# Performance work log

Hardware: AMD Instinct MI355X
Metric: run time of the kernel (lower is better)

The kernel has to match this reference:

```python
import jax, jax.numpy as jnp
import numpy as np

NUM_MODELS = 4
B = 16384
HIDDEN = 512
QDIM = 256
LAST_HIDDEN = 256
UW = 0.1          # uncertainty_weight
EPS = 1e-5        # LayerNorm eps (torch default)
FEAT_DIMS = [1024, 768, 512, 640]


def _linear(x, W, b):
    return x @ W.T + b


def _layernorm(h, g, b):
    mu = jnp.mean(h, axis=-1, keepdims=True)
    var = jnp.mean((h - mu) ** 2, axis=-1, keepdims=True)
    return (h - mu) * jax.lax.rsqrt(var + EPS) * g + b


def setup_inputs() -> dict:
    key = jax.random.key(0)
    ks = jax.random.split(key, 40)
    inp = {}
    for i, d in enumerate(FEAT_DIMS):
        inp[f"feat{i}"] = jax.random.normal(ks[i], (B, d), jnp.float32)
        inp[f"W_intra{i}"] = jax.random.normal(ks[4 + i], (HIDDEN, d), jnp.float32) / np.sqrt(d)
        inp[f"b_intra{i}"] = jnp.zeros((HIDDEN,), jnp.float32)
    inp["pred_scores"] = jax.random.uniform(ks[8], (B, NUM_MODELS), jnp.float32)
    inp["pred_vars"] = jax.random.uniform(ks[9], (B, NUM_MODELS), jnp.float32)
    inp["ln_g"] = jnp.ones((HIDDEN,), jnp.float32)
    inp["ln_b"] = jnp.zeros((HIDDEN,), jnp.float32)
    inp["Wq"] = jax.random.normal(ks[10], (QDIM, HIDDEN), jnp.float32) / np.sqrt(HIDDEN)
    inp["bq"] = jnp.zeros((QDIM,), jnp.float32)
    inp["Wk"] = jax.random.normal(ks[11], (QDIM, HIDDEN), jnp.float32) / np.sqrt(HIDDEN)
    inp["bk"] = jnp.zeros((QDIM,), jnp.float32)
    inp["Wv"] = jax.random.normal(ks[12], (QDIM, HIDDEN), jnp.float32) / np.sqrt(HIDDEN)
    inp["bv"] = jnp.zeros((QDIM,), jnp.float32)
    d1 = NUM_MODELS * QDIM + NUM_MODELS
    inp["W1"] = jax.random.normal(ks[13], (LAST_HIDDEN, d1), jnp.float32) / np.sqrt(d1)
    inp["b1"] = jnp.zeros((LAST_HIDDEN,), jnp.float32)
    inp["Wfc"] = jax.random.normal(ks[14], (1, LAST_HIDDEN), jnp.float32) / np.sqrt(LAST_HIDDEN)
    inp["bfc"] = jnp.zeros((1,), jnp.float32)
    return inp


def _forward(feats, pred_scores, pred_vars, W_intras, b_intras,
             ln_g, ln_b, Wq, bq, Wk, bk, Wv, bv, W1, b1, Wfc, bfc):
    # per-model branch: Linear -> ReLU -> (dropout=id) -> ReLU -> LayerNorm
    hiddens = []
    for i in range(NUM_MODELS):
        h = jax.nn.relu(_linear(feats[i], W_intras[i], b_intras[i]))
        h = jax.nn.relu(h)  # second relu after dropout (identity in eval)
        hiddens.append(_layernorm(h, ln_g, ln_b))
    H = jnp.stack(hiddens, axis=1)  # (B, M, HIDDEN)

    # cross-attention with uncertainty; NOTE source bug: key = drop(q) => keys == queries
    q = jnp.einsum('bmh,qh->bmq', H, Wq) + bq          # (B, M, Q)
    k = q                                              # faithful to `key = self.drop(q)`
    v = jnp.einsum('bmh,qh->bmq', H, Wv) + bv          # (B, M, Q)

    scores = jnp.einsum('biq,bjq->bij', q, k)          # (B, M, M)
    vars_ = pred_vars[:, None, :] + pred_vars[:, :, None]  # vars[b,i,j] = v[b,j] + v[b,i]
    scores = jax.nn.softmax(scores - UW * vars_, axis=-1)
    z = jnp.einsum('bij,bjq->biq', scores, v).reshape(B, NUM_MODELS * QDIM)

    out = jnp.concatenate([z, pred_scores], axis=-1)
    out = _linear(out, W1, b1)
    logits = _linear(out, Wfc, bfc)
    return jax.nn.sigmoid(logits)  # (B, 1)


def reference(feat0, feat1, feat2, feat3,
              W_intra0, b_intra0, W_intra1, b_intra1,
              W_intra2, b_intra2, W_intra3, b_intra3,
              pred_scores, pred_vars, ln_g, ln_b,
              Wq, bq, Wk, bk, Wv, bv, W1, b1, Wfc, bfc):
    feats = [feat0, feat1, feat2, feat3]
    W_intras = [W_intra0, W_intra1, W_intra2, W_intra3]
    b_intras = [b_intra0, b_intra1, b_intra2, b_intra3]
    return _forward(feats, pred_scores, pred_vars, W_intras, b_intras,
                    ln_g, ln_b, Wq, bq, Wk, bk, Wv, bv, W1, b1, Wfc, bfc)
```

## Files before the change

### kernel.cpp

```cpp
#include <hip/hip_runtime.h>
#include <hip/hip_bf16.h>


typedef __bf16 bf16;
typedef __bf16 bf16x4_t __attribute__((ext_vector_type(4)));
typedef __bf16 bf16x8_t __attribute__((ext_vector_type(8)));
typedef float  f32x4_t  __attribute__((ext_vector_type(4)));

__device__ __forceinline__ bf16x8_t cvt8(f32x4_t a, f32x4_t b) {
  bf16x8_t r;
  r[0] = (bf16)a[0]; r[1] = (bf16)a[1]; r[2] = (bf16)a[2]; r[3] = (bf16)a[3];
  r[4] = (bf16)b[0]; r[5] = (bf16)b[1]; r[6] = (bf16)b[2]; r[7] = (bf16)b[3];
  return r;
}

__device__ __forceinline__ void gl_lds16(const void* g, void* l) {
  __builtin_amdgcn_global_load_lds(
      (const __attribute__((address_space(1))) void*)g,
      (__attribute__((address_space(3))) void*)l, 16, 0, 0);
}

#define SBAR()   __builtin_amdgcn_s_barrier()
#define SCHED0() __builtin_amdgcn_sched_barrier(0)

__device__ __forceinline__ bf16x8_t frag_b16(const bf16* Ts, int row, int c0) {
  const int byte = row * 64 + ((c0 ^ ((row >> 1) & 3)) << 4);
  return *(const bf16x8_t*)((const char*)Ts + byte);
}
__device__ __forceinline__ bf16x8_t frag_f32(const float* Ts, int row, int g) {
  const int p0 = (2 * g)     ^ (row & 7);
  const int p1 = (2 * g + 1) ^ (row & 7);
  f32x4_t lo = *(const f32x4_t*)((const char*)Ts + row * 128 + (p0 << 4));
  f32x4_t hi = *(const f32x4_t*)((const char*)Ts + row * 128 + (p1 << 4));
  return cvt8(lo, hi);
}

__device__ __forceinline__ void stage_f32_512(const float* __restrict__ src, int ld,
                                              int k0, float* lds) {
  const int l = threadIdx.x & 63;
  const int w = threadIdx.x >> 6;
#pragma unroll
  for (int j = 0; j < 2; ++j) {
    const int rb = w * 16 + j * 8;
    const int r  = rb + (l >> 3);
    const int q  = (l & 7) ^ (r & 7);
    gl_lds16(src + (size_t)r * ld + k0 + q * 4, (char*)lds + rb * 128);
  }
}
__device__ __forceinline__ void stage_b512x32(const bf16* __restrict__ src, int ld,
                                              int k0, bf16* lds) {
  const int l = threadIdx.x & 63;
  const int w = threadIdx.x >> 6;
#pragma unroll
  for (int j = 0; j < 4; ++j) {
    const int rb = w * 64 + j * 16;
    const int r  = rb + (l >> 2);
    const int sc = (l & 3) ^ ((r >> 1) & 3);
    gl_lds16(src + (size_t)r * ld + k0 + sc * 8, (char*)lds + rb * 64);
  }
}

__global__ __launch_bounds__(512) void intra_ln_kernel(
    const float* __restrict__ f0, const float* __restrict__ f1,
    const float* __restrict__ f2, const float* __restrict__ f3,
    const bf16* __restrict__ wb0, const bf16* __restrict__ wb1,
    const bf16* __restrict__ wb2, const bf16* __restrict__ wb3,
    const float* __restrict__ bb0, const float* __restrict__ bb1,
    const float* __restrict__ bb2, const float* __restrict__ bb3,
    const float* __restrict__ lng, const float* __restrict__ lnb,
    bf16* __restrict__ Hout) {
  __shared__ __align__(16) char lds[98304];
  const int bid  = blockIdx.x;
  const int p    = bid & 255, half = bid >> 8;
  const int px   = (p & 7) * 32 + (p >> 3);
  int z = px & 3, y = px >> 2;
  if (half) { z ^= 2; y += 64; }
  const float* fp; const bf16* wp; const float* bp; int K;
  switch (z) {
    case 0:  fp = f0; wp = wb0; bp = bb0; K = 1024; break;
    case 1:  fp = f1; wp = wb1; bp = bb1; K = 768;  break;
    case 2:  fp = f2; wp = wb2; bp = bb2; K = 512;  break;
    default: fp = f3; wp = wb3; bp = bb3; K = 640;  break;
  }
  const float* A = fp + (size_t)(y * 128) * K;
  const bf16*  B = wp;
  const int tid = threadIdx.x;
  const int lane = tid & 63;
  const int wid  = tid >> 6;
  const int wm = wid >> 2, wn = wid & 3;
  const int fr = lane & 15, g = lane >> 4;

  f32x4_t acc[4][8];
#pragma unroll
  for (int i = 0; i < 4; ++i)
#pragma unroll
    for (int j = 0; j < 8; ++j) acc[i][j] = (f32x4_t){0.f, 0.f, 0.f, 0.f};

  const int nt = K >> 5;
  char* buf0 = lds;
  char* buf1 = lds + 49152;
  auto stage = [&](int t, char* buf) {
    stage_f32_512(A, K, t * 32, (float*)buf);
    stage_b512x32(B, K, t * 32, (bf16*)(buf + 16384));
  };
  stage(0, buf0);
  stage(1, buf1);
  for (int t = 0; t < nt; ++t) {
    char* cur = (t & 1) ? buf1 : buf0;
    if (t + 1 < nt) asm volatile("s_waitcnt vmcnt(6)" ::: "memory");
    else            asm volatile("s_waitcnt vmcnt(0)" ::: "memory");
    SBAR(); SCHED0();
    __builtin_amdgcn_s_setprio(1);
    {
      const float* Af = (const float*)cur;
      const bf16*  Bb = (const bf16*)(cur + 16384);
      bf16x8_t ar[4], br[8];
#pragma unroll
      for (int mi = 0; mi < 4; ++mi) ar[mi] = frag_f32(Af, wm * 64 + mi * 16 + fr, g);
#pragma unroll
      for (int ni = 0; ni < 8; ++ni) br[ni] = frag_b16(Bb, wn * 128 + ni * 16 + fr, g);
#pragma unroll
      for (int mi = 0; mi < 4; ++mi)
#pragma unroll
        for (int ni = 0; ni < 8; ++ni)
          acc[mi][ni] = __builtin_amdgcn_mfma_f32_16x16x32_bf16(ar[mi], br[ni], acc[mi][ni], 0, 0, 0);
    }
    __builtin_amdgcn_s_setprio(0);
    SCHED0(); SBAR();
    if (t + 2 < nt) stage(t + 2, cur);
  }

  float* part  = (float*)lds;
  float* muinv = (float*)(lds + 4096);
  float bv8[8];
#pragma unroll
  for (int ni = 0; ni < 8; ++ni) bv8[ni] = bp[wn * 128 + ni * 16 + fr];
#pragma unroll
  for (int mi = 0; mi < 4; ++mi)
#pragma unroll
    for (int j = 0; j < 4; ++j) {
      float s = 0.f, s2 = 0.f;
#pragma unroll
      for (int ni = 0; ni < 8; ++ni) {
        float v = fmaxf(acc[mi][ni][j] + bv8[ni], 0.f);
        s += v; s2 += v * v;
      }
#pragma unroll
      for (int off = 1; off < 16; off <<= 1) {
        s += __shfl_xor(s, off); s2 += __shfl_xor(s2, off);
      }
      if (fr == 0) {
        const int rl = mi * 16 + 4 * g + j;
        part[(wid * 64 + rl) * 2]     = s;
        part[(wid * 64 + rl) * 2 + 1] = s2;
      }
    }
  __syncthreads();
  if (tid < 128) {
    const int wmt = tid >> 6, rl = tid & 63;
    float s = 0.f, s2 = 0.f;
#pragma unroll
    for (int q = 0; q < 4; ++q) {
      s  += part[((wmt * 4 + q) * 64 + rl) * 2];
      s2 += part[((wmt * 4 + q) * 64 + rl) * 2 + 1];
    }
    const float mu  = s * (1.f / 512.f);
    const float var = s2 * (1.f / 512.f) - mu * mu;
    muinv[tid * 2]     = mu;
    muinv[tid * 2 + 1] = rsqrtf(var + 1e-5f);
  }
  __syncthreads();
  float gg[8], be[8];
#pragma unroll
  for (int ni = 0; ni < 8; ++ni) {
    const int col = wn * 128 + ni * 16 + fr;
    gg[ni] = lng[col]; be[ni] = lnb[col];
  }
#pragma unroll
  for (int mi = 0; mi < 4; ++mi)
#pragma unroll
    for (int j = 0; j < 4; ++j) {
      const int row = wm * 64 + mi * 16 + 4 * g + j;
      const float mu  = muinv[row * 2];
      const float inv = muinv[row * 2 + 1];
      bf16* hp = Hout + (size_t)(y * 128 + row) * 2048 + z * 512;
#pragma unroll
      for (int ni = 0; ni < 8; ++ni) {
        float v = fmaxf(acc[mi][ni][j] + bv8[ni], 0.f);
        hp[wn * 128 + ni * 16 + fr] = (bf16)((v - mu) * inv * gg[ni] + be[ni]);
      }
    }
}

__device__ __forceinline__ void stage_b16(const bf16* __restrict__ src, int ld,
                                          int k0, bf16* lds) {
  const int l = threadIdx.x & 63;
  const int w = threadIdx.x >> 6;
#pragma unroll
  for (int j = 0; j < 2; ++j) {
    const int rb = w * 32 + j * 16;
    const int r  = rb + (l >> 2);
    const int sc = (l & 3) ^ ((r >> 1) & 3);
    gl_lds16(src + (size_t)r * ld + k0 + sc * 8, (char*)lds + rb * 64);
  }
}
__device__ __forceinline__ void stage_f32(const float* __restrict__ src, int ld,
                                          int k0, float* lds) {
  const int l = threadIdx.x & 63;
  const int w = threadIdx.x >> 6;
#pragma unroll
  for (int j = 0; j < 4; ++j) {
    const int rb = w * 32 + j * 8;
    const int r  = rb + (l >> 3);
    const int q  = (l & 7) ^ (r & 7);
    gl_lds16(src + (size_t)r * ld + k0 + q * 4, (char*)lds + rb * 128);
  }
}
__device__ __forceinline__ void mfma_deep0(const char* buf, f32x4_t acc[4][4]) {
  const int lane = threadIdx.x & 63;
  const int wid  = threadIdx.x >> 6;
  const int wm = wid >> 1, wn = wid & 1;
  const int fr = lane & 15, g = lane >> 4;
  const bf16*  Ab = (const bf16*)buf;
  const float* Bf = (const float*)(buf + 8192);
  bf16x8_t ar[4], br[4];
#pragma unroll
  for (int mi = 0; mi < 4; ++mi) ar[mi] = frag_b16(Ab, wm * 64 + mi * 16 + fr, g);
#pragma unroll
  for (int ni = 0; ni < 4; ++ni) br[ni] = frag_f32(Bf, wn * 64 + ni * 16 + fr, g);
#pragma unroll
  for (int mi = 0; mi < 4; ++mi)
#pragma unroll
    for (int ni = 0; ni < 4; ++ni)
      acc[mi][ni] = __builtin_amdgcn_mfma_f32_16x16x32_bf16(ar[mi], br[ni], acc[mi][ni], 0, 0, 0);
}
__device__ __forceinline__ void core_deep3_0(const void* A, int lda, const void* B,
                                             int ldb, int K, char* lds,
                                             f32x4_t acc[4][4]) {
  const int nt = K >> 5;
  auto stage = [&](int t, char* buf) {
    stage_b16((const bf16*)A, lda, t * 32, (bf16*)buf);
    stage_f32((const float*)B, ldb, t * 32, (float*)(buf + 8192));
  };
  stage(0, lds); stage(1, lds + 24576); stage(2, lds + 49152);
  int bsel = 0;
  for (int t = 0; t < nt; ++t) {
    const int ahead = nt - 1 - t;
    if (ahead >= 2)      asm volatile("s_waitcnt vmcnt(12)" ::: "memory");
    else if (ahead == 1) asm volatile("s_waitcnt vmcnt(6)"  ::: "memory");
    else                 asm volatile("s_waitcnt vmcnt(0)"  ::: "memory");
    SBAR(); SCHED0();
    __builtin_amdgcn_s_setprio(1);
    mfma_deep0(lds + bsel * 24576, acc);
    __builtin_amdgcn_s_setprio(0);
    SCHED0(); SBAR();
    if (t + 3 < nt) stage(t + 3, lds + bsel * 24576);
    bsel = (bsel == 2) ? 0 : bsel + 1;
  }
}
template<int RELU>
__device__ __forceinline__ void epi_bf16(f32x4_t acc[4][4], bf16* __restrict__ C, int ldc,
                                         const float* __restrict__ bias) {
  const int lane = threadIdx.x & 63;
  const int wid  = threadIdx.x >> 6;
  const int wm = wid >> 1, wn = wid & 1;
  const int fr = lane & 15;
  const int rb = wm * 64 + 4 * (lane >> 4);
  const int cb = wn * 64 + fr;
  float bv[4];
#pragma unroll
  for (int ni = 0; ni < 4; ++ni) bv[ni] = bias[cb + ni * 16];
#pragma unroll
  for (int mi = 0; mi < 4; ++mi)
#pragma unroll
    for (int j = 0; j < 4; ++j)
#pragma unroll
      for (int ni = 0; ni < 4; ++ni) {
        float val = acc[mi][ni][j] + bv[ni];
        if (RELU) val = fmaxf(val, 0.f);
        C[(size_t)(rb + mi * 16 + j) * ldc + cb + ni * 16] = (bf16)val;
      }
}

__global__ __launch_bounds__(256) void qv_kernel(
    const bf16* __restrict__ H, const float* __restrict__ Wq,
    const float* __restrict__ Wv, const float* __restrict__ bq,
    const float* __restrict__ bv, bf16* __restrict__ qvout) {
  __shared__ __align__(16) char lds[73728];
  const int bid = blockIdx.x;
  const int lid = (bid & 7) * 256 + (bid >> 3);
  const int x = lid & 3, y = lid >> 2;
  const float* Wsrc = (x < 2) ? Wq : Wv;
  f32x4_t acc[4][4];
#pragma unroll
  for (int i = 0; i < 4; ++i)
#pragma unroll
    for (int j = 0; j < 4; ++j) acc[i][j] = (f32x4_t){0.f, 0.f, 0.f, 0.f};
  core_deep3_0(H + (size_t)(y * 128) * 512, 512,
               Wsrc + (size_t)((x & 1) * 128) * 512, 512, 512, lds, acc);
  const float* bias = (x < 2) ? bq + x * 128 : bv + (x - 2) * 128;
  epi_bf16<0>(acc, qvout + (size_t)(y * 128) * 512 + x * 128, 512, bias);
}

__global__ __launch_bounds__(256) void w1_kernel(
    const bf16* __restrict__ zb, const float* __restrict__ W1,
    const float* __restrict__ b1, const float* __restrict__ ps,
    float* __restrict__ obuf) {
  __shared__ __align__(16) char lds[73728];
  const int bid = blockIdx.x;
  const int lid = (bid & 7) * 32 + (bid >> 3);
  const int x = lid & 1, y = lid >> 1;
  f32x4_t acc[4][4];
#pragma unroll
  for (int i = 0; i < 4; ++i)
#pragma unroll
    for (int j = 0; j < 4; ++j) acc[i][j] = (f32x4_t){0.f, 0.f, 0.f, 0.f};
  core_deep3_0(zb + (size_t)(y * 128) * 1024, 1024,
               W1 + (size_t)(x * 128) * 1028, 1028, 1024, lds, acc);

  const int lane = threadIdx.x & 63;
  const int wid  = threadIdx.x >> 6;
  const int wm = wid >> 1, wn = wid & 1;
  const int fr = lane & 15;
  const int rb = wm * 64 + 4 * (lane >> 4);
  const int cb = x * 128 + wn * 64 + fr;
  float bv[4], wt[4][4];
#pragma unroll
  for (int ni = 0; ni < 4; ++ni) {
    bv[ni] = b1[cb + ni * 16];
#pragma unroll
    for (int m = 0; m < 4; ++m) wt[ni][m] = W1[(size_t)(cb + ni * 16) * 1028 + 1024 + m];
  }
#pragma unroll
  for (int mi = 0; mi < 4; ++mi)
#pragma unroll
    for (int j = 0; j < 4; ++j) {
      const int r = y * 128 + rb + mi * 16 + j;
      f32x4_t psv = *(const f32x4_t*)(ps + (size_t)r * 4);
#pragma unroll
      for (int ni = 0; ni < 4; ++ni) {
        float val = acc[mi][ni][j] + bv[ni]
                  + psv[0] * wt[ni][0] + psv[1] * wt[ni][1]
                  + psv[2] * wt[ni][2] + psv[3] * wt[ni][3];
        obuf[(size_t)r * 256 + cb + ni * 16] = val;
      }
    }
}

__device__ __forceinline__ void cp8(bf16* d, const float* s) {
  f32x4_t x0 = *(const f32x4_t*)s;
  f32x4_t x1 = *(const f32x4_t*)(s + 4);
  *(bf16x8_t*)d = cvt8(x0, x1);
}
__global__ __launch_bounds__(256) void prep_kernel(
    const float* __restrict__ w0, const float* __restrict__ w1s,
    const float* __restrict__ w2, const float* __restrict__ w3,
    bf16* __restrict__ o0, bf16* __restrict__ o1,
    bf16* __restrict__ o2, bf16* __restrict__ o3) {
  const int t = blockIdx.x * 256 + threadIdx.x;
  if (t < 65536)       { size_t i = (size_t)t * 8;            cp8(o0 + i, w0 + i); }
  else if (t < 114688) { size_t i = (size_t)(t - 65536) * 8;  cp8(o1 + i, w1s + i); }
  else if (t < 147456) { size_t i = (size_t)(t - 114688) * 8; cp8(o2 + i, w2 + i); }
  else                 { size_t i = (size_t)(t - 147456) * 8; cp8(o3 + i, w3 + i); }
}

__global__ __launch_bounds__(256)
void attn_kernel(const bf16* __restrict__ qv, const float* __restrict__ pvars,
                 bf16* __restrict__ z) {
  const int b    = blockIdx.x * 4 + (threadIdx.x >> 6);
  const int lane = threadIdx.x & 63;
  float qf[4][4], vf[4][4];
#pragma unroll
  for (int i = 0; i < 4; ++i) {
    const bf16* row = qv + ((size_t)b * 4 + i) * 512;
    bf16x4_t qq = *(const bf16x4_t*)(row + lane * 4);
    bf16x4_t vv = *(const bf16x4_t*)(row + 256 + lane * 4);
#pragma unroll
    for (int c = 0; c < 4; ++c) { qf[i][c] = (float)qq[c]; vf[i][c] = (float)vv[c]; }
  }
  float s[4][4];
#pragma unroll
  for (int i = 0; i < 4; ++i)
#pragma unroll
    for (int j = 0; j < 4; ++j)
      s[i][j] = qf[i][0] * qf[j][0] + qf[i][1] * qf[j][1] + qf[i][2] * qf[j][2] + qf[i][3] * qf[j][3];
#pragma unroll
  for (int off = 1; off < 64; off <<= 1)
#pragma unroll
    for (int i = 0; i < 4; ++i)
#pragma unroll
      for (int j = 0; j < 4; ++j) s[i][j] += __shfl_xor(s[i][j], off);

  float var4[4];
#pragma unroll
  for (int m = 0; m < 4; ++m) var4[m] = pvars[(size_t)b * 4 + m];
  float w[4][4];
#pragma unroll
  for (int i = 0; i < 4; ++i) {
    float t[4]; float mx = -1e30f;
#pragma unroll
    for (int j = 0; j < 4; ++j) { t[j] = s[i][j] - 0.1f * (var4[i] + var4[j]); mx = fmaxf(mx, t[j]); }
    float sum = 0.f;
#pragma unroll
    for (int j = 0; j < 4; ++j) { t[j] = expf(t[j] - mx); sum += t[j]; }
    const float is = 1.f / sum;
#pragma unroll
    for (int j = 0; j < 4; ++j) w[i][j] = t[j] * is;
  }
#pragma unroll
  for (int i = 0; i < 4; ++i) {
    bf16x4_t zo;
#pragma unroll
    for (int c = 0; c < 4; ++c) {
      float zf = w[i][0] * vf[0][c] + w[i][1] * vf[1][c] + w[i][2] * vf[2][c] + w[i][3] * vf[3][c];
      zo[c] = (bf16)zf;
    }
    *(bf16x4_t*)(z + ((size_t)b * 4 + i) * 256 + lane * 4) = zo;
  }
}

__global__ __launch_bounds__(256)
void fc_kernel(const float* __restrict__ o, const float* __restrict__ wfc,
               const float* __restrict__ bfc, float* __restrict__ out) {
  const int b    = blockIdx.x * 4 + (threadIdx.x >> 6);
  const int lane = threadIdx.x & 63;
  f32x4_t ov = *(const f32x4_t*)(o + (size_t)b * 256 + lane * 4);
  f32x4_t wv = *(const f32x4_t*)(wfc + lane * 4);
  float p = ov[0] * wv[0] + ov[1] * wv[1] + ov[2] * wv[2] + ov[3] * wv[3];
#pragma unroll
  for (int off = 1; off < 64; off <<= 1) p += __shfl_xor(p, off);
  if (lane == 0) {
    const float lg = p + bfc[0];
    out[b] = 1.f / (1.f + expf(-lg));
  }
}

extern "C" void kernel_launch(void* const* d_in, const int* in_sizes, int n_in,
                              void* d_out, int out_size, void* d_ws, size_t ws_size,
                              hipStream_t stream) {
  (void)in_sizes; (void)n_in; (void)out_size; (void)ws_size;
  const float* feat[4] = {(const float*)d_in[0], (const float*)d_in[3],
                          (const float*)d_in[6], (const float*)d_in[9]};
  const float* Wi[4]   = {(const float*)d_in[1], (const float*)d_in[4],
                          (const float*)d_in[7], (const float*)d_in[10]};
  const float* bi[4]   = {(const float*)d_in[2], (const float*)d_in[5],
                          (const float*)d_in[8], (const float*)d_in[11]};
  const float* ps  = (const float*)d_in[12];
  const float* pv  = (const float*)d_in[13];
  const float* lng = (const float*)d_in[14];
  const float* lnb = (const float*)d_in[15];
  const float* Wq  = (const float*)d_in[16];
  const float* bq  = (const float*)d_in[17];
  const float* Wv  = (const float*)d_in[20];
  const float* bvp = (const float*)d_in[21];
  const float* W1  = (const float*)d_in[22];
  const float* b1  = (const float*)d_in[23];
  const float* Wfc = (const float*)d_in[24];
  const float* bfc = (const float*)d_in[25];

  char* ws = (char*)d_ws;
  const size_t MB = 1024 * 1024;
  bf16*  hbuf  = (bf16*)ws;
  bf16*  zbuf  = (bf16*)ws;
  float* obuf  = (float*)(ws + 32 * MB);
  bf16*  wb0   = (bf16*)(ws + 64 * MB);
  bf16*  wb1   = (bf16*)(ws + 65 * MB);
  bf16*  wb2   = (bf16*)(ws + 65 * MB + 786432);
  bf16*  wb3   = (bf16*)(ws + 66 * MB + 262144);
  bf16*  qvout = (bf16*)(ws + 64 * MB);

  hipLaunchKernelGGL(prep_kernel, dim3(736), dim3(256), 0, stream,
                     Wi[0], Wi[1], Wi[2], Wi[3], wb0, wb1, wb2, wb3);
  hipLaunchKernelGGL(intra_ln_kernel, dim3(512), dim3(512), 0, stream,
                     feat[0], feat[1], feat[2], feat[3],
                     wb0, wb1, wb2, wb3, bi[0], bi[1], bi[2], bi[3],
                     lng, lnb, hbuf);
  hipLaunchKernelGGL(qv_kernel, dim3(2048), dim3(256), 0, stream,
                     hbuf, Wq, Wv, bq, bvp, qvout);
  hipLaunchKernelGGL(attn_kernel, dim3(16384 / 4), dim3(256), 0, stream, qvout, pv, zbuf);
  hipLaunchKernelGGL(w1_kernel, dim3(256), dim3(256), 0, stream, zbuf, W1, b1, ps, obuf);
  hipLaunchKernelGGL(fc_kernel, dim3(16384 / 4), dim3(256), 0, stream, obuf, Wfc, bfc, (float*)d_out);
}
```

Measured before the change: 237.9 us.

## Convert fp32 A tile to bf16 in registers before LDS, triple-buffer weights

The fp32 activation tile is now loaded into registers, converted to bf16 and written to a small double-buffered LDS region, instead of being copied as fp32 via direct global-to-LDS loads and converted on every fragment read. Weight tiles move to a three-slot ring buffer so each prefetch lands in a different slot from the one being read. This halves the LDS footprint and read traffic for A and drops repeated conversions, at the cost of register-staged loads that add VGPR pressure and an extra lgkmcnt wait, plus a larger total LDS allocation.

```diff
diff --git a/kernel.cpp b/kernel.cpp
--- a/kernel.cpp
+++ b/kernel.cpp
@@ -35,18 +35,6 @@
   return cvt8(lo, hi);
 }
 
-__device__ __forceinline__ void stage_f32_512(const float* __restrict__ src, int ld,
-                                              int k0, float* lds) {
-  const int l = threadIdx.x & 63;
-  const int w = threadIdx.x >> 6;
-#pragma unroll
-  for (int j = 0; j < 2; ++j) {
-    const int rb = w * 16 + j * 8;
-    const int r  = rb + (l >> 3);
-    const int q  = (l & 7) ^ (r & 7);
-    gl_lds16(src + (size_t)r * ld + k0 + q * 4, (char*)lds + rb * 128);
-  }
-}
 __device__ __forceinline__ void stage_b512x32(const bf16* __restrict__ src, int ld,
                                               int k0, bf16* lds) {
   const int l = threadIdx.x & 63;
@@ -69,7 +57,8 @@
     const float* __restrict__ bb2, const float* __restrict__ bb3,
     const float* __restrict__ lng, const float* __restrict__ lnb,
     bf16* __restrict__ Hout) {
-  __shared__ __align__(16) char lds[98304];
+  __shared__ __align__(16) char lds[114688];
+
   const int bid  = blockIdx.x;
   const int p    = bid & 255, half = bid >> 8;
   const int px   = (p & 7) * 32 + (p >> 3);
@@ -90,6 +79,10 @@
   const int wm = wid >> 2, wn = wid & 3;
   const int fr = lane & 15, g = lane >> 4;
 
+  const int srow = tid >> 2, sq = tid & 3;
+  const float* Af = A + (size_t)srow * K + sq * 8;
+  const int abyte = srow * 64 + ((sq ^ ((srow >> 1) & 3)) << 4);
+
   f32x4_t acc[4][8];
 #pragma unroll
   for (int i = 0; i < 4; ++i)
@@ -97,38 +90,55 @@
     for (int j = 0; j < 8; ++j) acc[i][j] = (f32x4_t){0.f, 0.f, 0.f, 0.f};
 
   const int nt = K >> 5;
-  char* buf0 = lds;
-  char* buf1 = lds + 49152;
-  auto stage = [&](int t, char* buf) {
-    stage_f32_512(A, K, t * 32, (float*)buf);
-    stage_b512x32(B, K, t * 32, (bf16*)(buf + 16384));
-  };
-  stage(0, buf0);
-  stage(1, buf1);
-  for (int t = 0; t < nt; ++t) {
-    char* cur = (t & 1) ? buf1 : buf0;
-    if (t + 1 < nt) asm volatile("s_waitcnt vmcnt(6)" ::: "memory");
-    else            asm volatile("s_waitcnt vmcnt(0)" ::: "memory");
-    SBAR(); SCHED0();
-    __builtin_amdgcn_s_setprio(1);
-    {
-      const float* Af = (const float*)cur;
-      const bf16*  Bb = (const bf16*)(cur + 16384);
-      bf16x8_t ar[4], br[8];
-#pragma unroll
-      for (int mi = 0; mi < 4; ++mi) ar[mi] = frag_f32(Af, wm * 64 + mi * 16 + fr, g);
-#pragma unroll
-      for (int ni = 0; ni < 8; ++ni) br[ni] = frag_b16(Bb, wn * 128 + ni * 16 + fr, g);
-#pragma unroll
-      for (int mi = 0; mi < 4; ++mi)
-#pragma unroll
-        for (int ni = 0; ni < 8; ++ni)
-          acc[mi][ni] = __builtin_amdgcn_mfma_f32_16x16x32_bf16(ar[mi], br[ni], acc[mi][ni], 0, 0, 0);
-    }
-    __builtin_amdgcn_s_setprio(0);
-    SCHED0(); SBAR();
-    if (t + 2 < nt) stage(t + 2, cur);
-  }
+
+  stage_b512x32(B, K, 0, (bf16*)(lds));
+  f32x4_t aA0 = *(const f32x4_t*)(Af + 0);
+  f32x4_t aA1 = *(const f32x4_t*)(Af + 4);
+  stage_b512x32(B, K, 32, (bf16*)(lds + 32768));
+  f32x4_t aB0, aB1;
+
+  int bcur = 0;
+#define INTRA_ITER(T, C0, C1, N0, N1)                                         \
+  {                                                                           \
+    const int t_ = (T);                                                       \
+    if (t_ < nt - 1) asm volatile("s_waitcnt vmcnt(4)" ::: "memory");         \
+    else             asm volatile("s_waitcnt vmcnt(0)" ::: "memory");         \
+    *(bf16x8_t*)(lds + 98304 + (t_ & 1) * 8192 + abyte) = cvt8(C0, C1);       \
+    asm volatile("s_waitcnt lgkmcnt(0)" ::: "memory");                        \
+    SBAR(); SCHED0();                                                         \
+    if (t_ + 1 < nt) {                                                        \
+      N0 = *(const f32x4_t*)(Af + (t_ + 1) * 32);                             \
+      N1 = *(const f32x4_t*)(Af + (t_ + 1) * 32 + 4);                         \
+    }                                                                         \
+    SCHED0();                                                                 \
+    __builtin_amdgcn_s_setprio(1);                                            \
+    {                                                                         \
+      const bf16* Ac = (const bf16*)(lds + 98304 + (t_ & 1) * 8192);          \
+      const bf16* Bc = (const bf16*)(lds + bcur * 32768);                     \
+      bf16x8_t ar[4], br[8];                                                  \
+      _Pragma("unroll")                                                       \
+      for (int mi = 0; mi < 4; ++mi) ar[mi] = frag_b16(Ac, wm * 64 + mi * 16 + fr, g); \
+      _Pragma("unroll")                                                       \
+      for (int ni = 0; ni < 8; ++ni) br[ni] = frag_b16(Bc, wn * 128 + ni * 16 + fr, g); \
+      _Pragma("unroll")                                                       \
+      for (int mi = 0; mi < 4; ++mi)                                          \
+        _Pragma("unroll")                                                     \
+        for (int ni = 0; ni < 8; ++ni)                                        \
+          acc[mi][ni] = __builtin_amdgcn_mfma_f32_16x16x32_bf16(ar[mi], br[ni], acc[mi][ni], 0, 0, 0); \
+    }                                                                         \
+    __builtin_amdgcn_s_setprio(0);                                            \
+    SCHED0(); SBAR();                                                         \
+    const int bn_ = (bcur == 2) ? 0 : bcur + 1;          \
+    const int b2_ = (bn_ == 2) ? 0 : bn_ + 1;           \
+    if (t_ + 2 < nt) stage_b512x32(B, K, (t_ + 2) * 32, (bf16*)(lds + b2_ * 32768)); \
+    bcur = bn_;                                                               \
+  }
+
+  for (int t = 0; t < nt; t += 2) {
+    INTRA_ITER(t,     aA0, aA1, aB0, aB1)
+    INTRA_ITER(t + 1, aB0, aB1, aA0, aA1)
+  }
+#undef INTRA_ITER
 
   float* part  = (float*)lds;
   float* muinv = (float*)(lds + 4096);
```

Measured after the change: 228.7 us. 1.04x faster.

## Double block size in intra_ln kernel and triple-buffer weight staging

Applied to the files above, without the earlier changes.

The fused intra-linear + LayerNorm kernel now runs 1024 threads (16 waves) per block instead of 512, so each wave computes a 64x64 tile rather than 64x128, which halves accumulator registers per wave. Weight tiles are triple-buffered and feature tiles double-buffered in a 128 KB LDS allocation. Loads for the next steps are issued before the wait, with the vmcnt counts adjusted to match. This aims to raise latency hiding and overlap of global loads with MFMA work, at the cost of more LDS, barrier overhead across more waves, and lower per-wave fragment reuse.

```diff
diff --git a/kernel.cpp b/kernel.cpp
--- a/kernel.cpp
+++ b/kernel.cpp
@@ -35,32 +35,7 @@
   return cvt8(lo, hi);
 }
 
-__device__ __forceinline__ void stage_f32_512(const float* __restrict__ src, int ld,
-                                              int k0, float* lds) {
-  const int l = threadIdx.x & 63;
-  const int w = threadIdx.x >> 6;
-#pragma unroll
-  for (int j = 0; j < 2; ++j) {
-    const int rb = w * 16 + j * 8;
-    const int r  = rb + (l >> 3);
-    const int q  = (l & 7) ^ (r & 7);
-    gl_lds16(src + (size_t)r * ld + k0 + q * 4, (char*)lds + rb * 128);
-  }
-}
-__device__ __forceinline__ void stage_b512x32(const bf16* __restrict__ src, int ld,
-                                              int k0, bf16* lds) {
-  const int l = threadIdx.x & 63;
-  const int w = threadIdx.x >> 6;
-#pragma unroll
-  for (int j = 0; j < 4; ++j) {
-    const int rb = w * 64 + j * 16;
-    const int r  = rb + (l >> 2);
-    const int sc = (l & 3) ^ ((r >> 1) & 3);
-    gl_lds16(src + (size_t)r * ld + k0 + sc * 8, (char*)lds + rb * 64);
-  }
-}
-
-__global__ __launch_bounds__(512) void intra_ln_kernel(
+__global__ __launch_bounds__(1024, 4) void intra_ln_kernel(
     const float* __restrict__ f0, const float* __restrict__ f1,
     const float* __restrict__ f2, const float* __restrict__ f3,
     const bf16* __restrict__ wb0, const bf16* __restrict__ wb1,
@@ -69,7 +44,8 @@
     const float* __restrict__ bb2, const float* __restrict__ bb3,
     const float* __restrict__ lng, const float* __restrict__ lnb,
     bf16* __restrict__ Hout) {
-  __shared__ __align__(16) char lds[98304];
+  __shared__ __align__(16) char lds[131072];
+
   const int bid  = blockIdx.x;
   const int p    = bid & 255, half = bid >> 8;
   const int px   = (p & 7) * 32 + (p >> 3);
@@ -84,65 +60,79 @@
   }
   const float* A = fp + (size_t)(y * 128) * K;
   const bf16*  B = wp;
-  const int tid = threadIdx.x;
+  const int tid  = threadIdx.x;
   const int lane = tid & 63;
   const int wid  = tid >> 6;
-  const int wm = wid >> 2, wn = wid & 3;
+  const int wm = wid >> 3, wn = wid & 7;
   const int fr = lane & 15, g = lane >> 4;
 
-  f32x4_t acc[4][8];
+  f32x4_t acc[4][4];
 #pragma unroll
   for (int i = 0; i < 4; ++i)
 #pragma unroll
-    for (int j = 0; j < 8; ++j) acc[i][j] = (f32x4_t){0.f, 0.f, 0.f, 0.f};
+    for (int j = 0; j < 4; ++j) acc[i][j] = (f32x4_t){0.f, 0.f, 0.f, 0.f};
 
   const int nt = K >> 5;
-  char* buf0 = lds;
-  char* buf1 = lds + 49152;
-  auto stage = [&](int t, char* buf) {
-    stage_f32_512(A, K, t * 32, (float*)buf);
-    stage_b512x32(B, K, t * 32, (bf16*)(buf + 16384));
+
+  auto stageA = [&](int t) {
+    const int rb = wid * 8;
+    const int r  = rb + (lane >> 3);
+    const int q  = (lane & 7) ^ (r & 7);
+    gl_lds16(A + (size_t)r * K + t * 32 + q * 4,
+             lds + 98304 + (t & 1) * 16384 + rb * 128);
   };
-  stage(0, buf0);
-  stage(1, buf1);
+  auto stageB = [&](int t) {
+#pragma unroll
+    for (int j = 0; j < 2; ++j) {
+      const int rb = wid * 32 + j * 16;
+      const int r  = rb + (lane >> 2);
+      const int sc = (lane & 3) ^ ((r >> 1) & 3);
+      gl_lds16(B + (size_t)r * K + t * 32 + sc * 8,
+               lds + (t % 3) * 32768 + rb * 64);
+    }
+  };
+
+  stageA(0); stageB(0); stageB(1);
   for (int t = 0; t < nt; ++t) {
-    char* cur = (t & 1) ? buf1 : buf0;
-    if (t + 1 < nt) asm volatile("s_waitcnt vmcnt(6)" ::: "memory");
-    else            asm volatile("s_waitcnt vmcnt(0)" ::: "memory");
+    if (t + 1 < nt) stageA(t + 1);
+    if (t + 2 < nt) stageB(t + 2);
+    const int rem = ((t + 1 < nt) ? 3 : 0) + ((t + 2 < nt) ? 2 : 0);
+    if (rem == 5)      asm volatile("s_waitcnt vmcnt(5)" ::: "memory");
+    else if (rem == 3) asm volatile("s_waitcnt vmcnt(3)" ::: "memory");
+    else               asm volatile("s_waitcnt vmcnt(0)" ::: "memory");
     SBAR(); SCHED0();
     __builtin_amdgcn_s_setprio(1);
     {
-      const float* Af = (const float*)cur;
-      const bf16*  Bb = (const bf16*)(cur + 16384);
-      bf16x8_t ar[4], br[8];
-#pragma unroll
-      for (int mi = 0; mi < 4; ++mi) ar[mi] = frag_f32(Af, wm * 64 + mi * 16 + fr, g);
-#pragma unroll
-      for (int ni = 0; ni < 8; ++ni) br[ni] = frag_b16(Bb, wn * 128 + ni * 16 + fr, g);
+      const float* Ac = (const float*)(lds + 98304 + (t & 1) * 16384);
+      const bf16*  Bc = (const bf16*)(lds + (t % 3) * 32768);
+      bf16x8_t ar[4], br[4];
+#pragma unroll
+      for (int mi = 0; mi < 4; ++mi) ar[mi] = frag_f32(Ac, wm * 64 + mi * 16 + fr, g);
+#pragma unroll
+      for (int ni = 0; ni < 4; ++ni) br[ni] = frag_b16(Bc, wn * 64 + ni * 16 + fr, g);
 #pragma unroll
       for (int mi = 0; mi < 4; ++mi)
 #pragma unroll
-        for (int ni = 0; ni < 8; ++ni)
+        for (int ni = 0; ni < 4; ++ni)
           acc[mi][ni] = __builtin_amdgcn_mfma_f32_16x16x32_bf16(ar[mi], br[ni], acc[mi][ni], 0, 0, 0);
     }
     __builtin_amdgcn_s_setprio(0);
     SCHED0(); SBAR();
-    if (t + 2 < nt) stage(t + 2, cur);
   }
 
   float* part  = (float*)lds;
-  float* muinv = (float*)(lds + 4096);
-  float bv8[8];
-#pragma unroll
-  for (int ni = 0; ni < 8; ++ni) bv8[ni] = bp[wn * 128 + ni * 16 + fr];
+  float* muinv = (float*)(lds + 8192);
+  float bv4[4];
+#pragma unroll
+  for (int ni = 0; ni < 4; ++ni) bv4[ni] = bp[wn * 64 + ni * 16 + fr];
 #pragma unroll
   for (int mi = 0; mi < 4; ++mi)
 #pragma unroll
     for (int j = 0; j < 4; ++j) {
       float s = 0.f, s2 = 0.f;
 #pragma unroll
-      for (int ni = 0; ni < 8; ++ni) {
-        float v = fmaxf(acc[mi][ni][j] + bv8[ni], 0.f);
+      for (int ni = 0; ni < 4; ++ni) {
+        float v = fmaxf(acc[mi][ni][j] + bv4[ni], 0.f);
         s += v; s2 += v * v;
       }
 #pragma unroll
@@ -160,9 +150,9 @@
     const int wmt = tid >> 6, rl = tid & 63;
     float s = 0.f, s2 = 0.f;
 #pragma unroll
-    for (int q = 0; q < 4; ++q) {
-      s  += part[((wmt * 4 + q) * 64 + rl) * 2];
-      s2 += part[((wmt * 4 + q) * 64 + rl) * 2 + 1];
+    for (int q = 0; q < 8; ++q) {
+      s  += part[((wmt * 8 + q) * 64 + rl) * 2];
+      s2 += part[((wmt * 8 + q) * 64 + rl) * 2 + 1];
     }
     const float mu  = s * (1.f / 512.f);
     const float var = s2 * (1.f / 512.f) - mu * mu;
@@ -170,10 +160,10 @@
     muinv[tid * 2 + 1] = rsqrtf(var + 1e-5f);
   }
   __syncthreads();
-  float gg[8], be[8];
-#pragma unroll
-  for (int ni = 0; ni < 8; ++ni) {
-    const int col = wn * 128 + ni * 16 + fr;
+  float gg[4], be[4];
+#pragma unroll
+  for (int ni = 0; ni < 4; ++ni) {
+    const int col = wn * 64 + ni * 16 + fr;
     gg[ni] = lng[col]; be[ni] = lnb[col];
   }
 #pragma unroll
@@ -185,9 +175,9 @@
       const float inv = muinv[row * 2 + 1];
       bf16* hp = Hout + (size_t)(y * 128 + row) * 2048 + z * 512;
 #pragma unroll
-      for (int ni = 0; ni < 8; ++ni) {
-        float v = fmaxf(acc[mi][ni][j] + bv8[ni], 0.f);
-        hp[wn * 128 + ni * 16 + fr] = (bf16)((v - mu) * inv * gg[ni] + be[ni]);
+      for (int ni = 0; ni < 4; ++ni) {
+        float v = fmaxf(acc[mi][ni][j] + bv4[ni], 0.f);
+        hp[wn * 64 + ni * 16 + fr] = (bf16)((v - mu) * inv * gg[ni] + be[ni]);
       }
     }
 }
@@ -471,7 +461,7 @@
 
   hipLaunchKernelGGL(prep_kernel, dim3(736), dim3(256), 0, stream,
                      Wi[0], Wi[1], Wi[2], Wi[3], wb0, wb1, wb2, wb3);
-  hipLaunchKernelGGL(intra_ln_kernel, dim3(512), dim3(512), 0, stream,
+  hipLaunchKernelGGL(intra_ln_kernel, dim3(512), dim3(1024), 0, stream,
                      feat[0], feat[1], feat[2], feat[3],
                      wb0, wb1, wb2, wb3, bi[0], bi[1], bi[2], bi[3],
                      lng, lnb, hbuf);
```

Result: slower. 248.1 us (+4.3%).
